# Kernel tuning notes

Hardware: AMD Instinct MI355X
Metric: run time of the kernel (lower is better)

## Reference

```python
import jax, jax.numpy as jnp
import numpy as np

N = 20000        # nodes
E = 160000       # directed edges (before self loops)
NODE_DIM = 1287
HEADS = 4
C1, C2, C3 = 128, 256, 128
ACT_SLOPE = 0.15   # module's LeakyReLU between layers
GAT_SLOPE = 0.2    # PyG GATConv default negative_slope


def _gat_layer(x, src, dst, W, att_src, att_dst, bias, heads, out_dim, concat):
    # x: [N, in] ; W: [in, heads*out] ; att_*: [heads, out] ; bias: [heads*out] or [out]
    h = (x @ W).reshape(N, heads, out_dim)                      # [N, H, C]
    a_s = jnp.einsum('nhc,hc->nh', h, att_src)                  # [N, H]
    a_d = jnp.einsum('nhc,hc->nh', h, att_dst)                  # [N, H]
    e = jax.nn.leaky_relu(a_s[src] + a_d[dst], GAT_SLOPE)       # [Etot, H]
    # segment softmax over incoming edges of each dst node (self loops => no empty segments)
    m = jax.ops.segment_max(e, dst, num_segments=N)             # [N, H]
    w = jnp.exp(e - m[dst])
    den = jax.ops.segment_sum(w, dst, num_segments=N)           # [N, H]
    alpha = w / den[dst]                                        # [Etot, H]
    msg = h[src] * alpha[:, :, None]                            # [Etot, H, C]
    out = jax.ops.segment_sum(msg, dst, num_segments=N)         # [N, H, C]
    out = out.reshape(N, heads * out_dim) if concat else out.mean(axis=1)
    return out + bias


def setup_inputs() -> dict:
    key = jax.random.key(0)
    ks = jax.random.split(key, 22)
    s = 0.05
    x = jax.random.normal(ks[0], (N, NODE_DIM), jnp.float32)
    edge_index = jax.random.randint(ks[1], (2, E), 0, N, dtype=jnp.int64)
    inp = {
        'x': x, 'edge_index': edge_index,
        'W1': jax.random.normal(ks[2], (NODE_DIM, HEADS * C1), jnp.float32) * s,
        'as1': jax.random.normal(ks[3], (HEADS, C1), jnp.float32) * s,
        'ad1': jax.random.normal(ks[4], (HEADS, C1), jnp.float32) * s,
        'b1': jnp.zeros((HEADS * C1,), jnp.float32),
        'W2': jax.random.normal(ks[5], (HEADS * C1, HEADS * C2), jnp.float32) * s,
        'as2': jax.random.normal(ks[6], (HEADS, C2), jnp.float32) * s,
        'ad2': jax.random.normal(ks[7], (HEADS, C2), jnp.float32) * s,
        'b2': jnp.zeros((HEADS * C2,), jnp.float32),
        # conv3: 1024 -> 128, 1 head, no concat
        'W3': jax.random.normal(ks[8], (HEADS * C2, C3), jnp.float32) * s,
        'as3': jax.random.normal(ks[9], (1, C3), jnp.float32) * s,
        'ad3': jax.random.normal(ks[10], (1, C3), jnp.float32) * s,
        'b3': jnp.zeros((C3,), jnp.float32),
        # pre_fc: 128 -> 16
        'pw': jax.random.normal(ks[11], (C3, 16), jnp.float32) * s,
        'pb': jnp.zeros((16,), jnp.float32),
        # fc fallback: Linear(16,32) -> LeakyReLU(0.15) -> Linear(32,2)
        'f1w': jax.random.normal(ks[12], (16, 32), jnp.float32) * s,
        'f1b': jnp.zeros((32,), jnp.float32),
        'f2w': jax.random.normal(ks[13], (32, 2), jnp.float32) * s,
        'f2b': jnp.zeros((2,), jnp.float32),
    }
    return inp


def reference(x, edge_index, W1, as1, ad1, b1, W2, as2, ad2, b2,
              W3, as3, ad3, b3, pw, pb, f1w, f1b, f2w, f2b):
    loop = jnp.arange(N, dtype=edge_index.dtype)
    src = jnp.concatenate([edge_index[0], loop])   # PyG add_self_loops=True
    dst = jnp.concatenate([edge_index[1], loop])
    h = _gat_layer(x, src, dst, W1, as1, ad1, b1, HEADS, C1, True)
    h = jax.nn.leaky_relu(h, ACT_SLOPE)            # dropout = identity (eval)
    h = _gat_layer(h, src, dst, W2, as2, ad2, b2, HEADS, C2, True)
    h = jax.nn.leaky_relu(h, ACT_SLOPE)
    h = _gat_layer(h, src, dst, W3, as3, ad3, b3, 1, C3, False)
    h = jax.nn.leaky_relu(h, ACT_SLOPE)
    h = h @ pw + pb                                 # pre_fc (128 -> 16)
    h = jax.nn.leaky_relu(h @ f1w + f1b, ACT_SLOPE)
    return h @ f2w + f2b                            # [N, 2] logits
```

## Files before the change

kernel.cpp:

```cpp
#include <hip/hip_runtime.h>
#include <hip/hip_bf16.h>
#include <cstdint>
#include <cstddef>

#define LRELU(x, s) ((x) > 0.f ? (x) : (s) * (x))

typedef __attribute__((ext_vector_type(8))) short bf16x8;
typedef __attribute__((ext_vector_type(4))) float f32x4;

__device__ __forceinline__ float bflo(uint v) { return __uint_as_float(v << 16); }
__device__ __forceinline__ float bfhi(uint v) { return __uint_as_float(v & 0xffff0000u); }
__device__ __forceinline__ ushort f2bf(float f) {
  const uint u = __float_as_uint(f);
  return (ushort)((u + 0x7fffu + ((u >> 16) & 1u)) >> 16);
}

__device__ __forceinline__ void async16(const ushort* g, ushort* l) {
  __builtin_amdgcn_global_load_lds(
      (const __attribute__((address_space(1))) unsigned int*)g,
      (__attribute__((address_space(3))) unsigned int*)l, 16, 0, 0);
}

#define WAITCNT_VM(n) (0xF70 | (n))

__global__ void cast_pad_rows(const float* __restrict__ in, ushort* __restrict__ out,
                              int rows, int K, int Kp) {
  const int P4 = Kp >> 2;
  const long long idx = (long long)blockIdx.x * blockDim.x + threadIdx.x;
  if (idx >= (long long)rows * P4) return;
  const int r = (int)(idx / P4);
  const int c = ((int)(idx - (long long)r * P4)) << 2;
  const float* p = in + (size_t)r * K + c;
  float v0 = 0.f, v1 = 0.f, v2 = 0.f, v3 = 0.f;
  if (c + 3 < K) { v0 = p[0]; v1 = p[1]; v2 = p[2]; v3 = p[3]; }
  else {
    if (c + 0 < K) v0 = p[0];
    if (c + 1 < K) v1 = p[1];
    if (c + 2 < K) v2 = p[2];
    if (c + 3 < K) v3 = p[3];
  }
  uint2 o;
  o.x = (uint)f2bf(v0) | ((uint)f2bf(v1) << 16);
  o.y = (uint)f2bf(v2) | ((uint)f2bf(v3) << 16);
  *(uint2*)(out + (size_t)r * Kp + c) = o;
}

__global__ void cast_W_T(const float* __restrict__ W, ushort* __restrict__ Wt,
                         int K, int Nn, int Kp) {
  __shared__ float tile[32][33];
  const int kt = blockIdx.x * 32;
  const int nt = blockIdx.y * 32;
  const int tx = threadIdx.x;
  const int ty = threadIdx.y;
  for (int r = ty; r < 32; r += 8) {
    const int k = kt + r, nn = nt + tx;
    tile[r][tx] = (k < K && nn < Nn) ? W[(size_t)k * Nn + nn] : 0.f;
  }
  __syncthreads();
  for (int r = ty; r < 32; r += 8) {
    const int nn = nt + r, k = kt + tx;
    if (nn < Nn && k < Kp) Wt[(size_t)nn * Kp + k] = f2bf(tile[tx][r]);
  }
}

template <int TM>
__global__ __launch_bounds__(256) void gemm_bf16(
    const ushort* __restrict__ A, const ushort* __restrict__ Bt, ushort* __restrict__ C,
    int M, int N, int Kp,
    const float* __restrict__ AS, const float* __restrict__ AD,
    float* __restrict__ asb, float* __restrict__ adb, int H, int headC) {
  constexpr int MI = TM / 32;
  constexpr int LPG = (TM == 128) ? 4 : 3;
  __shared__ ushort sA[2 * TM * 32];
  __shared__ ushort sB[2 * 128 * 32];
  const int tid = threadIdx.x;
  const int wave = tid >> 6;
  const int lane = tid & 63;
  const int tilesN = N >> 7;
  const int nwg = gridDim.x;
  const int q8 = nwg >> 3, r8 = nwg & 7;
  const int xcd = blockIdx.x & 7;
  const int lid = blockIdx.x >> 3;
  const int wg = (xcd < r8 ? xcd * (q8 + 1) : r8 * (q8 + 1) + (xcd - r8) * q8) + lid;
  const int bx = wg % tilesN;
  const int by = wg / tilesN;
  const int wrow = (wave >> 1) * (TM / 2);
  const int wcol = (wave & 1) * 64;
  const int quad = lane >> 4;
  const int ml = lane & 15;

  const int seg = (((lane & 3) ^ ((lane >> 3) & 3)) * 8);
  const int rB0 = wave * 32 + (lane >> 2);
  const int gB0 = bx * 128 + rB0;
  const ushort* pB0 = Bt + (size_t)gB0 * Kp + seg;
  const ushort* pB1 = Bt + (size_t)(gB0 + 16) * Kp + seg;
  ushort* lB0 = &sB[(wave * 32) * 32];
  ushort* lB1 = &sB[(wave * 32 + 16) * 32];
  const ushort *pA0, *pA1;
  ushort *lA0, *lA1;
  if constexpr (TM == 128) {
    const int r0 = wave * 32 + (lane >> 2);
    pA0 = A + (size_t)min(by * TM + r0, M - 1) * Kp + seg;
    pA1 = A + (size_t)min(by * TM + r0 + 16, M - 1) * Kp + seg;
    lA0 = &sA[(wave * 32) * 32];
    lA1 = &sA[(wave * 32 + 16) * 32];
  } else {
    const int r0 = wave * 16 + (lane >> 2);
    pA0 = A + (size_t)min(by * TM + r0, M - 1) * Kp + seg;
    pA1 = nullptr;
    lA0 = &sA[(wave * 16) * 32];
    lA1 = nullptr;
  }

  const int nIter = Kp >> 5;
  auto issue = [&](int it, int p) {
    const int k0 = it << 5;
    const int oa = p * TM * 32;
    const int ob_ = p * 128 * 32;
    async16(pA0 + k0, lA0 + oa);
    if constexpr (TM == 128) async16(pA1 + k0, lA1 + oa);
    async16(pB0 + k0, lB0 + ob_);
    async16(pB1 + k0, lB1 + ob_);
  };

  f32x4 acc[MI][4];
#pragma unroll
  for (int mi = 0; mi < MI; mi++)
#pragma unroll
    for (int ni = 0; ni < 4; ni++)
#pragma unroll
      for (int e = 0; e < 4; e++) acc[mi][ni][e] = 0.f;

  const int rq = (quad ^ ((ml >> 1) & 3)) * 8;

  issue(0, 0);
  if (nIter > 1) issue(1, 1);
  int p = 0;
  for (int it = 0; it < nIter; ++it) {
    if (it + 1 < nIter) __builtin_amdgcn_s_waitcnt(WAITCNT_VM(LPG));
    else __builtin_amdgcn_s_waitcnt(WAITCNT_VM(0));
    __builtin_amdgcn_s_barrier();
    const ushort* bA = &sA[p * TM * 32];
    const ushort* bB = &sB[p * 128 * 32];
    bf16x8 af[MI], bfr[4];
#pragma unroll
    for (int mi = 0; mi < MI; mi++)
      af[mi] = *(const bf16x8*)&bA[(wrow + mi * 16 + ml) * 32 + rq];
#pragma unroll
    for (int ni = 0; ni < 4; ni++)
      bfr[ni] = *(const bf16x8*)&bB[(wcol + ni * 16 + ml) * 32 + rq];
#pragma unroll
    for (int mi = 0; mi < MI; mi++)
#pragma unroll
      for (int ni = 0; ni < 4; ni++)
        acc[mi][ni] = __builtin_amdgcn_mfma_f32_16x16x32_bf16(af[mi], bfr[ni], acc[mi][ni], 0, 0, 0);
    if (it + 2 < nIter) {
      __builtin_amdgcn_s_barrier();
      issue(it + 2, p);
    }
    p ^= 1;
  }

#pragma unroll
  for (int mi = 0; mi < MI; mi++) {
#pragma unroll
    for (int r = 0; r < 4; r++) {
      const int row = by * TM + wrow + mi * 16 + quad * 4 + r;
      if (row < M) {
#pragma unroll
        for (int ni = 0; ni < 4; ni++) {
          const int col = bx * 128 + wcol + ni * 16 + ml;
          C[(size_t)row * N + col] = f2bf(acc[mi][ni][r]);
        }
      }
    }
  }

  if (asb != nullptr) {
    float asv[4], adv[4];
#pragma unroll
    for (int ni = 0; ni < 4; ni++) {
      const int col = bx * 128 + wcol + ni * 16 + ml;
      asv[ni] = AS[col];
      adv[ni] = AD[col];
    }
    const int hh = (bx * 128 + wcol) / headC;
#pragma unroll
    for (int mi = 0; mi < MI; mi++) {
#pragma unroll
      for (int r = 0; r < 4; r++) {
        float ps = acc[mi][0][r] * asv[0] + acc[mi][1][r] * asv[1] +
                   acc[mi][2][r] * asv[2] + acc[mi][3][r] * asv[3];
        float pd = acc[mi][0][r] * adv[0] + acc[mi][1][r] * adv[1] +
                   acc[mi][2][r] * adv[2] + acc[mi][3][r] * adv[3];
#pragma unroll
        for (int off = 1; off < 16; off <<= 1) {
          ps += __shfl_xor(ps, off);
          pd += __shfl_xor(pd, off);
        }
        if (ml == 0) {
          const int row = by * TM + wrow + mi * 16 + quad * 4 + r;
          if (row < M) {
            atomicAdd(&asb[row * H + hh], ps);
            atomicAdd(&adb[row * H + hh], pd);
          }
        }
      }
    }
  }
}

__global__ void count_deg(const int* __restrict__ dst, int E, int* __restrict__ deg) {
  const int t = blockIdx.x * blockDim.x + threadIdx.x;
  if (t < E) atomicAdd(&deg[dst[t]], 1);
}

__global__ __launch_bounds__(1024) void scan_kernel(const int* __restrict__ deg,
                                                    int* __restrict__ rowptr,
                                                    int* __restrict__ cursor, int n) {
  __shared__ int swsum[16];
  __shared__ int carry_s;
  const int t = threadIdx.x;
  const int wv = t >> 6, lane = t & 63;
  if (t == 0) carry_s = 0;
  __syncthreads();
  for (int base = 0; base < n; base += 1024) {
    const int i = base + t;
    const int v = (i < n) ? (deg[i] + 1) : 0;
    int sc = v;
#pragma unroll
    for (int off = 1; off < 64; off <<= 1) {
      const int u = __shfl_up(sc, off);
      if (lane >= off) sc += u;
    }
    if (lane == 63) swsum[wv] = sc;
    __syncthreads();
    if (t < 16) {
      int x = swsum[t];
#pragma unroll
      for (int off = 1; off < 16; off <<= 1) {
        const int u = __shfl_up(x, off);
        if (t >= off) x += u;
      }
      swsum[t] = x;
    }
    __syncthreads();
    const int incl = sc + (wv == 0 ? 0 : swsum[wv - 1]) + carry_s;
    if (i < n) { rowptr[i + 1] = incl; cursor[i] = incl - v; }
    if (base == 0 && t == 0) rowptr[0] = 0;
    __syncthreads();
    if (t == 0) carry_s += swsum[15];
    __syncthreads();
  }
}

__global__ void scatter_edges(const int* __restrict__ esrc, const int* __restrict__ edst,
                              int E, int Etot, int* __restrict__ cursor,
                              int* __restrict__ csr_src) {
  const int t = blockIdx.x * blockDim.x + threadIdx.x;
  if (t >= Etot) return;
  int s, d;
  if (t < E) { s = esrc[t]; d = edst[t]; } else { s = t - E; d = s; }
  const int pos = atomicAdd(&cursor[d], 1);
  csr_src[pos] = s;
}

template <int H, int C>
__global__ __launch_bounds__(256) void gat_agg_wave(
    const ushort* __restrict__ hb, const int* __restrict__ rowptr,
    const int* __restrict__ csr_src, const float* __restrict__ a_s,
    const float* __restrict__ a_d, const float* __restrict__ bias,
    ushort* __restrict__ outb, float act_slope, int Nn) {
  constexpr int HC = H * C;
  constexpr int NU = HC / 2;
  constexpr int UPT = NU / 256;
  const int n = blockIdx.x * 4 + (threadIdx.x >> 6);
  const int lane = threadIdx.x & 63;
  if (n >= Nn) return;
  float ad_n[H];
#pragma unroll
  for (int h = 0; h < H; h++) ad_n[h] = a_d[n * H + h];
  const int start = rowptr[n], end = rowptr[n + 1];
  f32x4 acc[UPT][2];
#pragma unroll
  for (int q = 0; q < UPT; q++)
#pragma unroll
    for (int u = 0; u < 2; u++)
#pragma unroll
      for (int e = 0; e < 4; e++) acc[q][u][e] = 0.f;
  float den[H];
#pragma unroll
  for (int h = 0; h < H; h++) den[h] = 0.f;

  for (int base = start; base < end; base += 64) {
    const int cnt = min(64, end - base);
    int s = 0;
    float w[H];
#pragma unroll
    for (int h = 0; h < H; h++) w[h] = 0.f;
    if (lane < cnt) {
      s = csr_src[base + lane];
      float asv[H];
      if constexpr (H == 4) {
        const float4 t4 = *(const float4*)(a_s + s * 4);
        asv[0] = t4.x; asv[1] = t4.y; asv[2] = t4.z; asv[3] = t4.w;
      } else {
        asv[0] = a_s[s];
      }
#pragma unroll
      for (int h = 0; h < H; h++) {
        float lg = asv[h] + ad_n[h];
        lg = LRELU(lg, 0.2f);
        w[h] = __expf(lg);
        den[h] += w[h];
      }
    }
    for (int j = 0; j < cnt; j++) {
      const int sj = __shfl(s, j);
      float wj[H];
#pragma unroll
      for (int h = 0; h < H; h++) wj[h] = __shfl(w[h], j);
      const uint4* hp = (const uint4*)(hb + (size_t)sj * HC);
#pragma unroll
      for (int q = 0; q < UPT; q++) {
        const int e0 = q * 512 + 8 * lane;
        const uint4 v = hp[q * 64 + lane];
        const float wq = wj[e0 / C];
        acc[q][0][0] += wq * bflo(v.x);
        acc[q][0][1] += wq * bfhi(v.x);
        acc[q][0][2] += wq * bflo(v.y);
        acc[q][0][3] += wq * bfhi(v.y);
        acc[q][1][0] += wq * bflo(v.z);
        acc[q][1][1] += wq * bfhi(v.z);
        acc[q][1][2] += wq * bflo(v.w);
        acc[q][1][3] += wq * bfhi(v.w);
      }
    }
  }
#pragma unroll
  for (int h = 0; h < H; h++) {
#pragma unroll
    for (int off = 1; off < 64; off <<= 1) den[h] += __shfl_xor(den[h], off);
    den[h] = 1.f / den[h];
  }
#pragma unroll
  for (int q = 0; q < UPT; q++) {
    const int e0 = q * 512 + 8 * lane;
    const float iv = den[e0 / C];
    const float4 ba = *(const float4*)(bias + e0);
    const float4 bb = *(const float4*)(bias + e0 + 4);
    const float o0 = LRELU(acc[q][0][0] * iv + ba.x, act_slope);
    const float o1 = LRELU(acc[q][0][1] * iv + ba.y, act_slope);
    const float o2 = LRELU(acc[q][0][2] * iv + ba.z, act_slope);
    const float o3 = LRELU(acc[q][0][3] * iv + ba.w, act_slope);
    const float o4 = LRELU(acc[q][1][0] * iv + bb.x, act_slope);
    const float o5 = LRELU(acc[q][1][1] * iv + bb.y, act_slope);
    const float o6 = LRELU(acc[q][1][2] * iv + bb.z, act_slope);
    const float o7 = LRELU(acc[q][1][3] * iv + bb.w, act_slope);
    uint4 o;
    o.x = (uint)f2bf(o0) | ((uint)f2bf(o1) << 16);
    o.y = (uint)f2bf(o2) | ((uint)f2bf(o3) << 16);
    o.z = (uint)f2bf(o4) | ((uint)f2bf(o5) << 16);
    o.w = (uint)f2bf(o6) | ((uint)f2bf(o7) << 16);
    ((uint4*)outb)[(size_t)n * (NU / 4) + q * 64 + lane] = o;
  }
}

__global__ __launch_bounds__(64) void gat_agg3_mlp(
    const ushort* __restrict__ hb, const int* __restrict__ rowptr,
    const int* __restrict__ csr_src, const float* __restrict__ a_s,
    const float* __restrict__ a_d, const float* __restrict__ b3,
    const float* __restrict__ pw, const float* __restrict__ pb,
    const float* __restrict__ f1w, const float* __restrict__ f1b,
    const float* __restrict__ f2w, const float* __restrict__ f2b,
    float* __restrict__ out) {
  const int n = blockIdx.x;
  const int tid = threadIdx.x;
  __shared__ float sx[128];
  __shared__ float s1[16];
  __shared__ float s2[32];
  const float ad_n = a_d[n];
  const int start = rowptr[n], end = rowptr[n + 1];
  float2 acc = make_float2(0.f, 0.f);
  float den = 0.f;
  for (int base = start; base < end; base += 64) {
    const int cnt = min(64, end - base);
    int s = 0;
    float w = 0.f;
    if (tid < cnt) {
      s = csr_src[base + tid];
      float lg = a_s[s] + ad_n;
      lg = LRELU(lg, 0.2f);
      w = __expf(lg);
      den += w;
    }
    for (int j = 0; j < cnt; j++) {
      const int sj = __shfl(s, j);
      const float wj = __shfl(w, j);
      const uint v = ((const uint*)(hb + (size_t)sj * 128))[tid];
      acc.x += wj * bflo(v);
      acc.y += wj * bfhi(v);
    }
  }
#pragma unroll
  for (int off = 1; off < 64; off <<= 1) den += __shfl_xor(den, off);
  const float iv = 1.f / den;
  sx[2 * tid]     = LRELU(acc.x * iv + b3[2 * tid], 0.15f);
  sx[2 * tid + 1] = LRELU(acc.y * iv + b3[2 * tid + 1], 0.15f);
  __syncthreads();
  if (tid < 16) {
    float a = pb[tid];
    for (int c = 0; c < 128; c++) a += sx[c] * pw[c * 16 + tid];
    s1[tid] = a;
  }
  __syncthreads();
  if (tid < 32) {
    float a = f1b[tid];
    for (int c = 0; c < 16; c++) a += s1[c] * f1w[c * 32 + tid];
    s2[tid] = LRELU(a, 0.15f);
  }
  __syncthreads();
  if (tid < 2) {
    float a = f2b[tid];
    for (int c = 0; c < 32; c++) a += s2[c] * f2w[c * 2 + tid];
    out[(size_t)n * 2 + tid] = a;
  }
}

extern "C" void kernel_launch(void* const* d_in, const int* in_sizes, int n_in,
                              void* d_out, int out_size, void* d_ws, size_t ws_size,
                              hipStream_t stream) {
  const float* x   = (const float*)d_in[0];
  const int* ei    = (const int*)d_in[1];
  const float* W1  = (const float*)d_in[2];
  const float* as1 = (const float*)d_in[3];
  const float* ad1 = (const float*)d_in[4];
  const float* b1  = (const float*)d_in[5];
  const float* W2  = (const float*)d_in[6];
  const float* as2 = (const float*)d_in[7];
  const float* ad2 = (const float*)d_in[8];
  const float* b2  = (const float*)d_in[9];
  const float* W3  = (const float*)d_in[10];
  const float* as3 = (const float*)d_in[11];
  const float* ad3 = (const float*)d_in[12];
  const float* b3  = (const float*)d_in[13];
  const float* pw  = (const float*)d_in[14];
  const float* pb  = (const float*)d_in[15];
  const float* f1w = (const float*)d_in[16];
  const float* f1b = (const float*)d_in[17];
  const float* f2w = (const float*)d_in[18];
  const float* f2b = (const float*)d_in[19];
  float* out = (float*)d_out;

  const int N = in_sizes[0] / 1287;
  const int E = in_sizes[1] / 2;
  const int Etot = E + N;
  const int* esrc = ei;
  const int* edst = ei + E;
  const int K1 = 1287, K1p = 1312;

  char* ws = (char*)d_ws;
  size_t off = 0;
  auto alloc = [&](size_t bytes) -> void* {
    void* p = ws + off;
    off = (off + bytes + 255) & ~(size_t)255;
    return p;
  };
  ushort* hb  = (ushort*)alloc((size_t)N * 1024 * 2);
  ushort* ob  = (ushort*)alloc((size_t)N * 1024 * 2);
  ushort* xb  = (ushort*)alloc((size_t)N * K1p * 2);
  ushort* W1t = (ushort*)alloc((size_t)512 * K1p * 2);
  ushort* W2t = (ushort*)alloc((size_t)1024 * 512 * 2);
  ushort* W3t = (ushort*)alloc((size_t)128 * 1024 * 2);
  float* av   = (float*)alloc((size_t)N * 8 * sizeof(float));
  int* deg    = (int*)alloc((size_t)N * sizeof(int));
  int* rowptr = (int*)alloc((size_t)(N + 1) * sizeof(int));
  int* cursor = (int*)alloc((size_t)N * sizeof(int));
  int* csr    = (int*)alloc((size_t)Etot * sizeof(int));
  float* asb = av;
  float* adb = av + (size_t)N * 4;

  hipMemsetAsync(deg, 0, (size_t)N * sizeof(int), stream);
  count_deg<<<(E + 255) / 256, 256, 0, stream>>>(edst, E, deg);
  scan_kernel<<<1, 1024, 0, stream>>>(deg, rowptr, cursor, N);
  scatter_edges<<<(Etot + 255) / 256, 256, 0, stream>>>(esrc, edst, E, Etot, cursor, csr);

  {
    const long long nx = (long long)N * (K1p / 4);
    cast_pad_rows<<<(int)((nx + 255) / 256), 256, 0, stream>>>(x, xb, N, K1, K1p);
    cast_W_T<<<dim3(K1p / 32, (512 + 31) / 32), dim3(32, 8), 0, stream>>>(W1, W1t, K1, 512, K1p);
    cast_W_T<<<dim3(512 / 32, 1024 / 32), dim3(32, 8), 0, stream>>>(W2, W2t, 512, 1024, 512);
    cast_W_T<<<dim3(1024 / 32, 128 / 32), dim3(32, 8), 0, stream>>>(W3, W3t, 1024, 128, 1024);
  }

  const int tilesM = (N + 127) / 128;
  const int tilesM64 = (N + 63) / 64;
  const int aggBlocks = (N + 3) / 4;

  {
    const int H = 4, C = 128, HC = 512;
    hipMemsetAsync(av, 0, (size_t)N * 8 * sizeof(float), stream);
    gemm_bf16<128><<<tilesM * (HC / 128), 256, 0, stream>>>(xb, W1t, hb, N, HC, K1p,
                                                            as1, ad1, asb, adb, H, C);
    gat_agg_wave<4, 128><<<aggBlocks, 256, 0, stream>>>(hb, rowptr, csr, asb, adb,
                                                        b1, ob, 0.15f, N);
  }
  {
    const int H = 4, C = 256, HC = 1024;
    hipMemsetAsync(av, 0, (size_t)N * 8 * sizeof(float), stream);
    gemm_bf16<128><<<tilesM * (HC / 128), 256, 0, stream>>>(ob, W2t, hb, N, HC, 512,
                                                            as2, ad2, asb, adb, H, C);
    gat_agg_wave<4, 256><<<aggBlocks, 256, 0, stream>>>(hb, rowptr, csr, asb, adb,
                                                        b2, ob, 0.15f, N);
  }
  {
    const int HC = 128;
    hipMemsetAsync(av, 0, (size_t)N * 8 * sizeof(float), stream);
    gemm_bf16<64><<<tilesM64 * (HC / 128), 256, 0, stream>>>(ob, W3t, hb, N, HC, 1024,
                                                             as3, ad3, asb, adb, 1, 128);
    gat_agg3_mlp<<<N, 64, 0, stream>>>(hb, rowptr, csr, asb, adb, b3,
                                       pw, pb, f1w, f1b, f2w, f2b, out);
  }
}
```

Measured before the change: 515.7 us.

## Add 128x256-tile 512-thread bf16 GEMM for the first two GAT layers

Adds a new GEMM kernel with a 128x256 output tile and 8 waves, each computing 64x64 with 16x16x32 MFMAs. It is used for the layer-1 and layer-2 projections in place of the 128x128 256-thread kernel. The wider tile means each A row tile is loaded half as often, and the kernel keeps the async LDS double buffering, the XCD-aware block remapping and the fused attention-score reduction. In exchange each block uses more LDS and registers and the grid is halved, which may lower occupancy and hurt tail balance.

```diff
diff --git a/kernel.cpp b/kernel.cpp
--- a/kernel.cpp
+++ b/kernel.cpp
@@ -60,6 +60,149 @@
   for (int r = ty; r < 32; r += 8) {
     const int nn = nt + r, k = kt + tx;
     if (nn < Nn && k < Kp) Wt[(size_t)nn * Kp + k] = f2bf(tile[tx][r]);
+  }
+}
+
+__global__ __launch_bounds__(512) void gemm_wide(
+    const ushort* __restrict__ A, const ushort* __restrict__ Bt, ushort* __restrict__ C,
+    int M, int N, int Kp,
+    const float* __restrict__ AS, const float* __restrict__ AD,
+    float* __restrict__ asb, float* __restrict__ adb, int H, int headC) {
+  __shared__ ushort smem[24576];
+  ushort* sA = smem;
+  ushort* sB = smem + 8192;
+  const int tid = threadIdx.x;
+  const int wave = tid >> 6;
+  const int lane = tid & 63;
+  const int tilesN = N >> 8;
+  const int nwg = gridDim.x;
+  const int q8 = nwg >> 3, r8 = nwg & 7;
+  const int xcd = blockIdx.x & 7;
+  const int lid = blockIdx.x >> 3;
+  const int wg = (xcd < r8 ? xcd * (q8 + 1) : r8 * (q8 + 1) + (xcd - r8) * q8) + lid;
+  const int bx = wg % tilesN;
+  const int by = wg / tilesN;
+  const int wr = wave >> 2;
+  const int wc = wave & 3;
+  const int wrow = wr * 64;
+  const int wcol = wc * 64;
+  const int quad = lane >> 4;
+  const int ml = lane & 15;
+  const int seg = (((lane & 3) ^ ((lane >> 3) & 3)) * 8);
+
+  const int rA = wave * 16 + (lane >> 2);
+  const ushort* pA = A + (size_t)min(by * 128 + rA, M - 1) * Kp + seg;
+  ushort* lA = &sA[(wave * 16) * 32];
+  const int rB = wave * 32 + (lane >> 2);
+  const ushort* pB0 = Bt + (size_t)(bx * 256 + rB) * Kp + seg;
+  const ushort* pB1 = Bt + (size_t)(bx * 256 + rB + 16) * Kp + seg;
+  ushort* lB0 = &sB[(wave * 32) * 32];
+  ushort* lB1 = &sB[(wave * 32 + 16) * 32];
+
+  const int nIter = Kp >> 5;
+  auto issue = [&](int it, int p) {
+    const int k0 = it << 5;
+    async16(pA + k0, lA + p * 4096);
+    async16(pB0 + k0, lB0 + p * 8192);
+    async16(pB1 + k0, lB1 + p * 8192);
+  };
+
+  f32x4 acc[4][4];
+#pragma unroll
+  for (int mi = 0; mi < 4; mi++)
+#pragma unroll
+    for (int ni = 0; ni < 4; ni++)
+#pragma unroll
+      for (int e = 0; e < 4; e++) acc[mi][ni][e] = 0.f;
+
+  const int rq = (quad ^ ((ml >> 1) & 3)) * 8;
+
+  issue(0, 0);
+  if (nIter > 1) issue(1, 1);
+  int p = 0;
+  for (int it = 0; it < nIter; ++it) {
+    if (it + 1 < nIter) __builtin_amdgcn_s_waitcnt(WAITCNT_VM(3));
+    else __builtin_amdgcn_s_waitcnt(WAITCNT_VM(0));
+    __builtin_amdgcn_s_barrier();
+    const ushort* bA = sA + p * 4096;
+    const ushort* bB = sB + p * 8192;
+    bf16x8 af[4], bfr[4];
+#pragma unroll
+    for (int mi = 0; mi < 4; mi++)
+      af[mi] = *(const bf16x8*)&bA[(wrow + mi * 16 + ml) * 32 + rq];
+#pragma unroll
+    for (int ni = 0; ni < 4; ni++)
+      bfr[ni] = *(const bf16x8*)&bB[(wcol + ni * 16 + ml) * 32 + rq];
+#pragma unroll
+    for (int mi = 0; mi < 4; mi++)
+#pragma unroll
+      for (int ni = 0; ni < 4; ni++)
+        acc[mi][ni] = __builtin_amdgcn_mfma_f32_16x16x32_bf16(af[mi], bfr[ni], acc[mi][ni], 0, 0, 0);
+    if (it + 2 < nIter) {
+      __builtin_amdgcn_s_barrier();
+      issue(it + 2, p);
+    }
+    p ^= 1;
+  }
+
+  ushort* sC = smem;
+  for (int h = 0; h < 2; ++h) {
+    __syncthreads();
+    if (wr == h) {
+#pragma unroll
+      for (int mi = 0; mi < 4; mi++)
+#pragma unroll
+        for (int r = 0; r < 4; r++) {
+          const int lr = mi * 16 + quad * 4 + r;
+#pragma unroll
+          for (int ni = 0; ni < 4; ni++)
+            sC[lr * 264 + wcol + ni * 16 + ml] = f2bf(acc[mi][ni][r]);
+        }
+    }
+    __syncthreads();
+#pragma unroll
+    for (int rd = 0; rd < 4; ++rd) {
+      const int idx = rd * 512 + tid;
+      const int lr = idx >> 5, c16 = idx & 31;
+      const int row = by * 128 + h * 64 + lr;
+      if (row < M) {
+        const uint4 v = *(const uint4*)&sC[lr * 264 + c16 * 8];
+        *(uint4*)(C + (size_t)row * N + bx * 256 + c16 * 8) = v;
+      }
+    }
+  }
+
+  if (asb != nullptr) {
+    float asv[4], adv[4];
+#pragma unroll
+    for (int ni = 0; ni < 4; ni++) {
+      const int col = bx * 256 + wcol + ni * 16 + ml;
+      asv[ni] = AS[col];
+      adv[ni] = AD[col];
+    }
+    const int hh = (bx * 256 + wcol) / headC;
+#pragma unroll
+    for (int mi = 0; mi < 4; mi++) {
+#pragma unroll
+      for (int r = 0; r < 4; r++) {
+        float ps = acc[mi][0][r] * asv[0] + acc[mi][1][r] * asv[1] +
+                   acc[mi][2][r] * asv[2] + acc[mi][3][r] * asv[3];
+        float pd = acc[mi][0][r] * adv[0] + acc[mi][1][r] * adv[1] +
+                   acc[mi][2][r] * adv[2] + acc[mi][3][r] * adv[3];
+#pragma unroll
+        for (int off = 1; off < 16; off <<= 1) {
+          ps += __shfl_xor(ps, off);
+          pd += __shfl_xor(pd, off);
+        }
+        if (ml == 0) {
+          const int row = by * 128 + wrow + mi * 16 + quad * 4 + r;
+          if (row < M) {
+            atomicAdd(&asb[row * H + hh], ps);
+            atomicAdd(&adb[row * H + hh], pd);
+          }
+        }
+      }
+    }
   }
 }
 
@@ -500,16 +643,16 @@
   {
     const int H = 4, C = 128, HC = 512;
     hipMemsetAsync(av, 0, (size_t)N * 8 * sizeof(float), stream);
-    gemm_bf16<128><<<tilesM * (HC / 128), 256, 0, stream>>>(xb, W1t, hb, N, HC, K1p,
-                                                            as1, ad1, asb, adb, H, C);
+    gemm_wide<<<tilesM * (HC / 256), 512, 0, stream>>>(xb, W1t, hb, N, HC, K1p,
+                                                       as1, ad1, asb, adb, H, C);
     gat_agg_wave<4, 128><<<aggBlocks, 256, 0, stream>>>(hb, rowptr, csr, asb, adb,
                                                         b1, ob, 0.15f, N);
   }
   {
     const int H = 4, C = 256, HC = 1024;
     hipMemsetAsync(av, 0, (size_t)N * 8 * sizeof(float), stream);
-    gemm_bf16<128><<<tilesM * (HC / 128), 256, 0, stream>>>(ob, W2t, hb, N, HC, 512,
-                                                            as2, ad2, asb, adb, H, C);
+    gemm_wide<<<tilesM * (HC / 256), 512, 0, stream>>>(ob, W2t, hb, N, HC, 512,
+                                                       as2, ad2, asb, adb, H, C);
     gat_agg_wave<4, 256><<<aggBlocks, 256, 0, stream>>>(hb, rowptr, csr, asb, adb,
                                                         b2, ob, 0.15f, N);
   }
```

Result: no change. 521.3 us (+1.1%).

## Move attention dot products out of GEMM epilogue into separate kernel; use readlane

Applied to the files above, without the earlier changes.

Takes the per-head attention-score reductions (shuffles plus atomics) out of the GEMM epilogue. They now run in a dedicated att_dots kernel that reads the bf16 projected features and writes scores directly, so the memsets and atomics are no longer needed. It also replaces __shfl broadcasts in the aggregation loops with readlane scalar broadcasts, which cuts LDS/permute traffic. In exchange it adds three kernel launches and re-reads the hidden features. The scores are now computed from bf16-rounded values rather than fp32 accumulators, a small numerical change.

```diff
diff --git a/kernel.cpp b/kernel.cpp
--- a/kernel.cpp
+++ b/kernel.cpp
@@ -63,12 +63,10 @@
   }
 }
 
-template <int TM>
+template <int TM, int TAG>
 __global__ __launch_bounds__(256) void gemm_bf16(
     const ushort* __restrict__ A, const ushort* __restrict__ Bt, ushort* __restrict__ C,
-    int M, int N, int Kp,
-    const float* __restrict__ AS, const float* __restrict__ AD,
-    float* __restrict__ asb, float* __restrict__ adb, int H, int headC) {
+    int M, int N, int Kp) {
   constexpr int MI = TM / 32;
   constexpr int LPG = (TM == 128) ? 4 : 3;
   __shared__ ushort sA[2 * TM * 32];
@@ -175,38 +173,40 @@
       }
     }
   }
-
-  if (asb != nullptr) {
-    float asv[4], adv[4];
-#pragma unroll
-    for (int ni = 0; ni < 4; ni++) {
-      const int col = bx * 128 + wcol + ni * 16 + ml;
-      asv[ni] = AS[col];
-      adv[ni] = AD[col];
-    }
-    const int hh = (bx * 128 + wcol) / headC;
-#pragma unroll
-    for (int mi = 0; mi < MI; mi++) {
-#pragma unroll
-      for (int r = 0; r < 4; r++) {
-        float ps = acc[mi][0][r] * asv[0] + acc[mi][1][r] * asv[1] +
-                   acc[mi][2][r] * asv[2] + acc[mi][3][r] * asv[3];
-        float pd = acc[mi][0][r] * adv[0] + acc[mi][1][r] * adv[1] +
-                   acc[mi][2][r] * adv[2] + acc[mi][3][r] * adv[3];
-#pragma unroll
-        for (int off = 1; off < 16; off <<= 1) {
-          ps += __shfl_xor(ps, off);
-          pd += __shfl_xor(pd, off);
-        }
-        if (ml == 0) {
-          const int row = by * TM + wrow + mi * 16 + quad * 4 + r;
-          if (row < M) {
-            atomicAdd(&asb[row * H + hh], ps);
-            atomicAdd(&adb[row * H + hh], pd);
-          }
-        }
-      }
-    }
+}
+
+template <int H, int C>
+__global__ __launch_bounds__(256) void att_dots(
+    const ushort* __restrict__ hb, const float* __restrict__ AS,
+    const float* __restrict__ AD, float* __restrict__ asb, float* __restrict__ adb,
+    int Nn) {
+  constexpr int HC = H * C;
+  constexpr int EPL = HC / 64;
+  constexpr int S = C / EPL;
+  const int n = blockIdx.x * 4 + (threadIdx.x >> 6);
+  const int lane = threadIdx.x & 63;
+  if (n >= Nn) return;
+  const int head = lane / S;
+  const int cbase = (lane % S) * EPL;
+  const ushort* row = hb + (size_t)n * HC + lane * EPL;
+  const float* as_h = AS + head * C;
+  const float* ad_h = AD + head * C;
+  float ps = 0.f, pd = 0.f;
+#pragma unroll
+  for (int j = 0; j < EPL; j += 2) {
+    const uint v = *(const uint*)(row + j);
+    const float lo = bflo(v), hi = bfhi(v);
+    ps += lo * as_h[cbase + j] + hi * as_h[cbase + j + 1];
+    pd += lo * ad_h[cbase + j] + hi * ad_h[cbase + j + 1];
+  }
+#pragma unroll
+  for (int off = 1; off < S; off <<= 1) {
+    ps += __shfl_xor(ps, off);
+    pd += __shfl_xor(pd, off);
+  }
+  if ((lane % S) == 0) {
+    asb[n * H + head] = ps;
+    adb[n * H + head] = pd;
   }
 }
 
@@ -316,10 +316,11 @@
       }
     }
     for (int j = 0; j < cnt; j++) {
-      const int sj = __shfl(s, j);
+      const int sj = __builtin_amdgcn_readlane(s, j);
       float wj[H];
 #pragma unroll
-      for (int h = 0; h < H; h++) wj[h] = __shfl(w[h], j);
+      for (int h = 0; h < H; h++)
+        wj[h] = __uint_as_float(__builtin_amdgcn_readlane(__float_as_uint(w[h]), j));
       const uint4* hp = (const uint4*)(hb + (size_t)sj * HC);
 #pragma unroll
       for (int q = 0; q < UPT; q++) {
@@ -395,8 +396,8 @@
       den += w;
     }
     for (int j = 0; j < cnt; j++) {
-      const int sj = __shfl(s, j);
-      const float wj = __shfl(w, j);
+      const int sj = __builtin_amdgcn_readlane(s, j);
+      const float wj = __uint_as_float(__builtin_amdgcn_readlane(__float_as_uint(w), j));
       const uint v = ((const uint*)(hb + (size_t)sj * 128))[tid];
       acc.x += wj * bflo(v);
       acc.y += wj * bfhi(v);
@@ -495,29 +496,26 @@
 
   const int tilesM = (N + 127) / 128;
   const int tilesM64 = (N + 63) / 64;
-  const int aggBlocks = (N + 3) / 4;
+  const int nodeBlocks = (N + 3) / 4;
 
   {
-    const int H = 4, C = 128, HC = 512;
-    hipMemsetAsync(av, 0, (size_t)N * 8 * sizeof(float), stream);
-    gemm_bf16<128><<<tilesM * (HC / 128), 256, 0, stream>>>(xb, W1t, hb, N, HC, K1p,
-                                                            as1, ad1, asb, adb, H, C);
-    gat_agg_wave<4, 128><<<aggBlocks, 256, 0, stream>>>(hb, rowptr, csr, asb, adb,
-                                                        b1, ob, 0.15f, N);
+    const int HC = 512;
+    gemm_bf16<128, 1><<<tilesM * (HC / 128), 256, 0, stream>>>(xb, W1t, hb, N, HC, K1p);
+    att_dots<4, 128><<<nodeBlocks, 256, 0, stream>>>(hb, as1, ad1, asb, adb, N);
+    gat_agg_wave<4, 128><<<nodeBlocks, 256, 0, stream>>>(hb, rowptr, csr, asb, adb,
+                                                         b1, ob, 0.15f, N);
   }
   {
-    const int H = 4, C = 256, HC = 1024;
-    hipMemsetAsync(av, 0, (size_t)N * 8 * sizeof(float), stream);
-    gemm_bf16<128><<<tilesM * (HC / 128), 256, 0, stream>>>(ob, W2t, hb, N, HC, 512,
-                                                            as2, ad2, asb, adb, H, C);
-    gat_agg_wave<4, 256><<<aggBlocks, 256, 0, stream>>>(hb, rowptr, csr, asb, adb,
-                                                        b2, ob, 0.15f, N);
+    const int HC = 1024;
+    gemm_bf16<128, 2><<<tilesM * (HC / 128), 256, 0, stream>>>(ob, W2t, hb, N, HC, 512);
+    att_dots<4, 256><<<nodeBlocks, 256, 0, stream>>>(hb, as2, ad2, asb, adb, N);
+    gat_agg_wave<4, 256><<<nodeBlocks, 256, 0, stream>>>(hb, rowptr, csr, asb, adb,
+                                                         b2, ob, 0.15f, N);
   }
   {
     const int HC = 128;
-    hipMemsetAsync(av, 0, (size_t)N * 8 * sizeof(float), stream);
-    gemm_bf16<64><<<tilesM64 * (HC / 128), 256, 0, stream>>>(ob, W3t, hb, N, HC, 1024,
-                                                             as3, ad3, asb, adb, 1, 128);
+    gemm_bf16<64, 3><<<tilesM64 * (HC / 128), 256, 0, stream>>>(ob, W3t, hb, N, HC, 1024);
+    att_dots<1, 128><<<nodeBlocks, 256, 0, stream>>>(hb, as3, ad3, asb, adb, N);
     gat_agg3_mlp<<<N, 64, 0, stream>>>(hb, rowptr, csr, asb, adb, b3,
                                        pw, pb, f1w, f1b, f2w, f2b, out);
   }
```

Result: faster. 479.0 us (-7.1%).
